# Kernel tuning notes

Hardware: AMD Instinct MI355X
Metric: run time of the kernel (lower is better)

## Reference

```python
import jax, jax.numpy as jnp
import numpy as np
from jax import lax

B, S, D, N_ORIG, GROUP_DIM, R = 8, 4096, 512, 4096, 64, 1024
EPS_MERGE = 1e-8
EPS_NORM = 1e-12  # F.normalize eps


def setup_inputs() -> dict:
    key = jax.random.key(0)
    k1, k2, k3 = jax.random.split(key, 3)
    x = jax.random.normal(k1, (B, S, D), dtype=jnp.float32)
    source = jax.random.normal(k2, (B, S, N_ORIG), dtype=jnp.float32)
    position_ids = jnp.arange(B * S, dtype=jnp.int32).reshape(B, S)
    # nn.Linear(dim, group_dim, bias=False) weight: (group_dim, dim)
    W = jax.random.normal(k3, (GROUP_DIM, D), dtype=jnp.float32) / np.sqrt(D)
    return {"x": x, "source": source, "position_ids": position_ids, "W": W, "r": R}


def _greedy_select(sim, r):
    """Greedy disjoint adjacent-pair selection; returns bool (S-1,) edge mask."""
    Sm1 = sim.shape[0]
    order = jnp.argsort(-sim, stable=True)  # matches torch.argsort(-sim, stable=True)

    def step(carry, p):
        used, sel, cnt = carry
        ok = (~used[p]) & (~used[p + 1]) & (cnt < r)
        used = used.at[p].set(used[p] | ok)
        used = used.at[p + 1].set(used[p + 1] | ok)
        sel = sel.at[p].set(ok)
        return (used, sel, cnt + ok.astype(jnp.int32)), None

    init = (jnp.zeros(Sm1 + 1, dtype=bool), jnp.zeros(Sm1, dtype=bool), jnp.int32(0))
    (_, sel, _), _ = lax.scan(step, init, order)
    return sel


def _merge_one(x, src, pos, sim, norms, r):
    Sl = x.shape[0]
    sel = _greedy_select(sim, r)  # sel[p] True => merge pair (p, p+1)
    w = norms[:, None]
    # weighted merge of adjacent pairs, written at position i = p
    merged = (w[:-1] * x[:-1] + w[1:] * x[1:]) / (w[:-1] + w[1:] + EPS_MERGE)
    x_out = jnp.concatenate([jnp.where(sel[:, None], merged, x[:-1]), x[-1:]], axis=0)
    src_out = src.at[:-1].add(jnp.where(sel[:, None], src[1:], 0.0))
    drop = jnp.concatenate([jnp.zeros(1, dtype=bool), sel])  # token p+1 dropped
    idx = jnp.arange(Sl)
    keep_order = jnp.argsort(jnp.where(drop, Sl + idx, idx))[: Sl - r]  # kept, in order
    return x_out[keep_order], src_out[keep_order], pos[keep_order]


def reference(x, source, position_ids, W, r):
    g = jnp.einsum("bsd,gd->bsg", x, W)  # group projection
    gnorms = jnp.linalg.norm(g, axis=-1)  # (B, S)
    g_unit = g / jnp.maximum(gnorms[..., None], EPS_NORM)
    sim = jnp.sum(g_unit[:, :-1] * g_unit[:, 1:], axis=-1)  # (B, S-1)
    merge = lambda xb, sb, pb, simb, nb: _merge_one(xb, sb, pb, simb, nb, r)
    return jax.vmap(merge)(x, source, position_ids, sim, gnorms)
```

## Files before the change

kernel.cpp:

```cpp
#include <hip/hip_runtime.h>
#include <hip/hip_bf16.h>
#include <stdint.h>

#define B_ 8
#define S_ 4096
#define D_ 512
#define G_ 64
#define R_ 1024
#define NO_ 4096
#define SO_ 3072
#define EPS_MERGE 1e-8f
#define EPS_NORM 1e-12f

typedef float f4v __attribute__((ext_vector_type(4)));

#define WS_G     0ull
#define WS_GN    8388608ull
#define WS_KEYS  8519680ull
#define WS_KEPT  8781824ull

__global__ __launch_bounds__(256) void k1_proj(const float* __restrict__ x,
                                               const float* __restrict__ W,
                                               float* __restrict__ g,
                                               float* __restrict__ gn) {
  __shared__ float xs[32][132];
  __shared__ float wc[32][68];
  const int tid = threadIdx.x;
  const int gt  = tid & 15;
  const int rt  = tid >> 4;
  const int rb  = blockIdx.x * 128;
  const int g0  = gt * 4;
  const int r0  = rt * 8;
  const int kq4 = (tid & 7) * 4;
  const int rl0 = tid >> 3;

  const float* xp[4];
  const float* wp[2];
#pragma unroll
  for (int i = 0; i < 4; ++i)
    xp[i] = &x[(size_t)(rb + rl0 + i * 32) * D_ + kq4];
#pragma unroll
  for (int i = 0; i < 2; ++i)
    wp[i] = &W[(size_t)(rl0 + i * 32) * D_ + kq4];

  float4 px[4], pw[2];
#pragma unroll
  for (int i = 0; i < 4; ++i) px[i] = *reinterpret_cast<const float4*>(xp[i]);
#pragma unroll
  for (int i = 0; i < 2; ++i) pw[i] = *reinterpret_cast<const float4*>(wp[i]);

  float acc[8][4];
#pragma unroll
  for (int r = 0; r < 8; ++r)
#pragma unroll
    for (int j = 0; j < 4; ++j) acc[r][j] = 0.f;

  for (int kc = 0; kc < 16; ++kc) {
    __syncthreads();
#pragma unroll
    for (int i = 0; i < 4; ++i) {
      const int rl = rl0 + i * 32;
      xs[kq4 + 0][rl] = px[i].x;
      xs[kq4 + 1][rl] = px[i].y;
      xs[kq4 + 2][rl] = px[i].z;
      xs[kq4 + 3][rl] = px[i].w;
    }
#pragma unroll
    for (int i = 0; i < 2; ++i) {
      const int gg = rl0 + i * 32;
      wc[kq4 + 0][gg] = pw[i].x;
      wc[kq4 + 1][gg] = pw[i].y;
      wc[kq4 + 2][gg] = pw[i].z;
      wc[kq4 + 3][gg] = pw[i].w;
    }
    if (kc < 15) {
      const int off = (kc + 1) * 32;
#pragma unroll
      for (int i = 0; i < 4; ++i)
        px[i] = *reinterpret_cast<const float4*>(xp[i] + off);
#pragma unroll
      for (int i = 0; i < 2; ++i)
        pw[i] = *reinterpret_cast<const float4*>(wp[i] + off);
    }
    __syncthreads();
#pragma unroll
    for (int k = 0; k < 32; ++k) {
      const float4 wv = *reinterpret_cast<const float4*>(&wc[k][g0]);
      const float4 xa = *reinterpret_cast<const float4*>(&xs[k][r0]);
      const float4 xb = *reinterpret_cast<const float4*>(&xs[k][r0 + 4]);
      const float xr[8] = {xa.x, xa.y, xa.z, xa.w, xb.x, xb.y, xb.z, xb.w};
#pragma unroll
      for (int r = 0; r < 8; ++r) {
        acc[r][0] = fmaf(xr[r], wv.x, acc[r][0]);
        acc[r][1] = fmaf(xr[r], wv.y, acc[r][1]);
        acc[r][2] = fmaf(xr[r], wv.z, acc[r][2]);
        acc[r][3] = fmaf(xr[r], wv.w, acc[r][3]);
      }
    }
  }
#pragma unroll
  for (int r = 0; r < 8; ++r) {
    const int row = rb + r0 + r;
    float4 v;
    v.x = acc[r][0]; v.y = acc[r][1]; v.z = acc[r][2]; v.w = acc[r][3];
    *reinterpret_cast<float4*>(&g[(size_t)row * G_ + g0]) = v;
    float ss = v.x * v.x + v.y * v.y + v.z * v.z + v.w * v.w;
    ss += __shfl_xor(ss, 1);
    ss += __shfl_xor(ss, 2);
    ss += __shfl_xor(ss, 4);
    ss += __shfl_xor(ss, 8);
    if (gt == 0) gn[row] = sqrtf(ss);
  }
}

__global__ __launch_bounds__(256) void k2_sim(const float* __restrict__ g,
                                              const float* __restrict__ gn,
                                              unsigned long long* __restrict__ prio) {
  const int wid = blockIdx.x * 4 + (threadIdx.x >> 6);
  const int lane = threadIdx.x & 63;
  if (wid >= B_ * (S_ - 1)) return;
  const int b = wid / (S_ - 1);
  const int e = wid - b * (S_ - 1);
  const size_t row = (size_t)b * S_ + e;
  const float a = g[row * G_ + lane];
  const float c = g[(row + 1) * G_ + lane];
  float p = a * c;
  p += __shfl_xor(p, 1);
  p += __shfl_xor(p, 2);
  p += __shfl_xor(p, 4);
  p += __shfl_xor(p, 8);
  p += __shfl_xor(p, 16);
  p += __shfl_xor(p, 32);
  if (lane == 0) {
    const float n0 = fmaxf(gn[row], EPS_NORM);
    const float n1 = fmaxf(gn[row + 1], EPS_NORM);
    const float sim = p / (n0 * n1);
    const unsigned int u = __float_as_uint(sim);
    const unsigned int m = (u & 0x80000000u) ? ~u : (u | 0x80000000u);
    prio[(size_t)b * S_ + e] =
        ((unsigned long long)m << 32) | (unsigned long long)(unsigned int)(4095 - e);
  }
}

__global__ __launch_bounds__(256) void k3_match(const unsigned long long* __restrict__ prio,
                                                unsigned int* __restrict__ kept) {
  __shared__ unsigned long long pr[4096];
  __shared__ unsigned int stw[258];
  __shared__ int hist[256];
  __shared__ int wsum[4];
  __shared__ int sh_flag;
  __shared__ int sh_need;
  __shared__ int sh_exact;
  __shared__ unsigned long long sh_prefix;
  __shared__ unsigned long long sh_tmin;
  __shared__ unsigned long long sh_tmax;

  const int tid = threadIdx.x;
  const int b = blockIdx.x;

#pragma unroll
  for (int j = 0; j < 16; ++j) {
    const int e = tid + j * 256;
    pr[e] = (e < 4095) ? prio[(size_t)b * S_ + e] : 0ull;
  }
  if (tid == 0) {
    stw[0] = 0xAAAAAAAAu;
    stw[257] = 0xAAAAAAAAu;
    sh_flag = 0; sh_need = R_; sh_prefix = 0ull;
    sh_exact = 0; sh_tmin = ~0ull; sh_tmax = 0ull;
  }
  stw[1 + tid] = (tid == 255) ? 0x80000000u : 0u;
  __syncthreads();

  unsigned int cl = 0, cr = 0;
#pragma unroll
  for (int j = 0; j < 16; ++j) {
    const int e = tid * 16 + j;
    const unsigned long long pe = pr[e];
    const bool L = (e == 0) || (pe > pr[e - 1]);
    const bool R = (e >= 4094) || (pe > pr[e + 1]);
    cl |= (L ? 1u : 0u) << (2 * j);
    cr |= (R ? 1u : 0u) << (2 * j);
  }

  for (;;) {
    __syncthreads();
    if (tid == 0) sh_flag = 0;
    __syncthreads();
    unsigned int u = stw[1 + tid];
    const unsigned int lw = stw[tid];
    const unsigned int rw = stw[2 + tid];
    const unsigned int linb = (lw >> 30) & 1u;
    const unsigned int loutb = (lw >> 31) & 1u;
    const unsigned int rinb = (rw & 1u) << 30;
    const unsigned int routb = ((rw >> 1) & 1u) << 30;
    bool changed = false;
    for (;;) {
      const unsigned int a = u & 0x55555555u;
      const unsigned int d = (u >> 1) & 0x55555555u;
      const unsigned int lin = (a << 2) | linb;
      const unsigned int lout = (d << 2) | loutb;
      const unsigned int rin = (a >> 2) | rinb;
      const unsigned int rout = (d >> 2) | routb;
      const unsigned int undec = ~(a | d) & 0x55555555u;
      const unsigned int nout = undec & (lin | rin);
      const unsigned int nin = undec & ~lin & ~rin & (lout | cl) & (rout | cr);
      if (!(nin | nout)) break;
      u |= nin | (nout << 1);
      changed = true;
    }
    if (changed) { stw[1 + tid] = u; sh_flag = 1; }
    __syncthreads();
    if (sh_flag == 0) break;
  }

  const unsigned int inw = stw[1 + tid] & 0x55555555u;

  int exitmode = 0;
#pragma unroll 1
  for (int level = 0; level < 8; ++level) {
    const int shift = 56 - 8 * level;
    __syncthreads();
    hist[tid] = 0;
    __syncthreads();
    const unsigned long long pref = sh_prefix;
#pragma unroll
    for (int j = 0; j < 16; ++j) {
      if (!((inw >> (2 * j)) & 1u)) continue;
      const unsigned long long p = pr[tid * 16 + j];
      const bool match = (level == 0) || ((p >> (shift + 8)) == (pref >> (shift + 8)));
      if (match) atomicAdd(&hist[(int)((p >> shift) & 255ull)], 1);
    }
    __syncthreads();
    if (tid < 64) {
      const int lane = tid;
      const int need = sh_need;
      const int h0 = hist[lane * 4 + 0], h1 = hist[lane * 4 + 1];
      const int h2 = hist[lane * 4 + 2], h3 = hist[lane * 4 + 3];
      const int gsum = h0 + h1 + h2 + h3;
      int s = gsum;
#pragma unroll
      for (int off = 1; off < 64; off <<= 1) {
        const int v = __shfl_down(s, off);
        if (lane + off < 64) s += v;
      }
      const int suffAbove = s - gsum;
      if (suffAbove < need && s >= need) {
        const int hh[4] = {h0, h1, h2, h3};
        int cum = suffAbove;
        for (int q = 3; q >= 0; --q) {
          cum += hh[q];
          if (cum >= need) {
            const int need2 = need - (cum - hh[q]);
            sh_prefix = pref | ((unsigned long long)(lane * 4 + q) << shift);
            sh_need = need2;
            if (need2 == hh[q]) sh_exact = 1;
            else if (need2 == 1) sh_exact = 2;
            break;
          }
        }
      }
    }
    __syncthreads();
    const int ex = sh_exact;
    if (ex) {
      exitmode = ex;
      const unsigned long long pref2 = sh_prefix;
      unsigned long long best = (ex == 1) ? ~0ull : 0ull;
#pragma unroll
      for (int j = 0; j < 16; ++j) {
        if (!((inw >> (2 * j)) & 1u)) continue;
        const unsigned long long p = pr[tid * 16 + j];
        if ((p >> shift) == (pref2 >> shift))
          best = (ex == 1) ? (best < p ? best : p) : (best > p ? best : p);
      }
#pragma unroll
      for (int off = 1; off < 64; off <<= 1) {
        const unsigned long long o = __shfl_xor(best, off);
        best = (ex == 1) ? (best < o ? best : o) : (best > o ? best : o);
      }
      if ((tid & 63) == 0) {
        if (ex == 1) atomicMin(&sh_tmin, best);
        else atomicMax(&sh_tmax, best);
      }
      __syncthreads();
      break;
    }
  }
  const unsigned long long thresh =
      (exitmode == 1) ? sh_tmin : (exitmode == 2) ? sh_tmax : sh_prefix;
  const unsigned int previnw = stw[tid] & 0x55555555u;

  int c = 0;
  unsigned int kpbits = 0;
#pragma unroll
  for (int j = 0; j < 16; ++j) {
    const int s = tid * 16 + j;
    bool selprev = false;
    if (s > 0) {
      const unsigned int ib =
          (j == 0) ? ((previnw >> 30) & 1u) : ((inw >> (2 * (j - 1))) & 1u);
      selprev = ib && (pr[s - 1] >= thresh);
    }
    if (!selprev) { kpbits |= 1u << j; ++c; }
  }
  const int lane = tid & 63, w = tid >> 6;
  int v = c;
#pragma unroll
  for (int off = 1; off < 64; off <<= 1) {
    const int t2 = __shfl_up(v, off);
    if (lane >= off) v += t2;
  }
  if (lane == 63) wsum[w] = v;
  __syncthreads();
  if (tid == 0) {
    int run = 0;
    for (int q = 0; q < 4; ++q) { const int t3 = wsum[q]; wsum[q] = run; run += t3; }
  }
  __syncthreads();
  int pos = (v - c) + wsum[w];
#pragma unroll
  for (int j = 0; j < 16; ++j) {
    if ((kpbits >> j) & 1u) {
      const int s = tid * 16 + j;
      const unsigned int m =
          (((inw >> (2 * j)) & 1u) && pr[s] >= thresh) ? 0x80000000u : 0u;
      kept[b * SO_ + pos] = (unsigned int)s | m;
      ++pos;
    }
  }
}

__global__ __launch_bounds__(256) void k45_gather(const float* __restrict__ src,
                                                  const float* __restrict__ x,
                                                  const float* __restrict__ gn,
                                                  const int* __restrict__ posid,
                                                  const unsigned int* __restrict__ kept,
                                                  float* __restrict__ outs,
                                                  float* __restrict__ outx,
                                                  float* __restrict__ outpos) {
  const int blk = blockIdx.x;
  const int b = blk / SO_;
  const int j = blk - b * SO_;
  const unsigned int ent = kept[b * SO_ + j];
  const int s = (int)(ent & 0x7FFFFFFFu);
  const bool m = (ent & 0x80000000u) != 0u;
  const size_t rrow = (size_t)b * S_ + s;
  const size_t orow = (size_t)b * SO_ + j;
  const size_t rin = rrow * NO_;
  const size_t rout = orow * NO_;
  const int t = threadIdx.x;

#pragma unroll
  for (int it = 0; it < 4; ++it) {
    const int f4 = t + it * 256;
    f4v a = __builtin_nontemporal_load(
        reinterpret_cast<const f4v*>(&src[rin + (size_t)f4 * 4]));
    if (m) {
      const f4v c2 = __builtin_nontemporal_load(
          reinterpret_cast<const f4v*>(&src[rin + NO_ + (size_t)f4 * 4]));
      a += c2;
    }
    __builtin_nontemporal_store(a, reinterpret_cast<f4v*>(&outs[rout + (size_t)f4 * 4]));
  }

  if (t < 128) {
    float4 a = *reinterpret_cast<const float4*>(&x[rrow * D_ + t * 4]);
    float4 o;
    if (m) {
      const float w0 = gn[rrow], w1 = gn[rrow + 1];
      const float4 c2 = *reinterpret_cast<const float4*>(&x[(rrow + 1) * D_ + t * 4]);
      const float den = w0 + w1 + EPS_MERGE;
      o.x = (w0 * a.x + w1 * c2.x) / den;
      o.y = (w0 * a.y + w1 * c2.y) / den;
      o.z = (w0 * a.z + w1 * c2.z) / den;
      o.w = (w0 * a.w + w1 * c2.w) / den;
    } else {
      o = a;
    }
    *reinterpret_cast<float4*>(&outx[orow * D_ + t * 4]) = o;
  }
  if (t == 0) outpos[orow] = (float)posid[rrow];
}

extern "C" void kernel_launch(void* const* d_in, const int* in_sizes, int n_in,
                              void* d_out, int out_size, void* d_ws, size_t ws_size,
                              hipStream_t stream) {
  (void)in_sizes; (void)n_in; (void)out_size; (void)ws_size;
  const float* x = (const float*)d_in[0];
  const float* src = (const float*)d_in[1];
  const int* posid = (const int*)d_in[2];
  const float* W = (const float*)d_in[3];

  char* ws = (char*)d_ws;
  float* g = (float*)(ws + WS_G);
  float* gn = (float*)(ws + WS_GN);
  unsigned long long* prio = (unsigned long long*)(ws + WS_KEYS);
  unsigned int* kept = (unsigned int*)(ws + WS_KEPT);

  float* outx = (float*)d_out;
  float* outs = outx + (size_t)B_ * SO_ * D_;
  float* outpos = outs + (size_t)B_ * SO_ * NO_;

  hipLaunchKernelGGL(k1_proj, dim3(256), dim3(256), 0, stream, x, W, g, gn);
  hipLaunchKernelGGL(k2_sim, dim3((B_ * (S_ - 1) + 3) / 4), dim3(256), 0, stream, g, gn, prio);
  hipLaunchKernelGGL(k3_match, dim3(B_), dim3(256), 0, stream, prio, kept);
  hipLaunchKernelGGL(k45_gather, dim3(B_ * SO_), dim3(256), 0, stream, src, x, gn,
                     posid, kept, outs, outx, outpos);
}
```

Measured before the change: 228.8 us.

## Fuse projection and similarity kernels, keep group projections in shared memory

Merges the projection GEMM and the adjacent-pair cosine similarity into one kernel. The projected tile stays in LDS, and one halo row from the next block is recomputed so edges at block boundaries can be scored locally. This removes the global write and read of the 8 MB g buffer and one kernel launch, at the cost of a small redundant row computation done by a few threads. It also switches the x loads and outx stores in the gather kernel to nontemporal access.

```diff
diff --git a/kernel.cpp b/kernel.cpp
--- a/kernel.cpp
+++ b/kernel.cpp
@@ -14,17 +14,18 @@
 
 typedef float f4v __attribute__((ext_vector_type(4)));
 
-#define WS_G     0ull
-#define WS_GN    8388608ull
-#define WS_KEYS  8519680ull
-#define WS_KEPT  8781824ull
-
-__global__ __launch_bounds__(256) void k1_proj(const float* __restrict__ x,
-                                               const float* __restrict__ W,
-                                               float* __restrict__ g,
-                                               float* __restrict__ gn) {
-  __shared__ float xs[32][132];
-  __shared__ float wc[32][68];
+#define WS_GN    0ull
+#define WS_KEYS  131072ull
+#define WS_KEPT  393216ull
+
+__global__ __launch_bounds__(256) void k12_proj_sim(const float* __restrict__ x,
+                                                    const float* __restrict__ W,
+                                                    float* __restrict__ gn,
+                                                    unsigned long long* __restrict__ prio) {
+  __shared__ union {
+    struct { float xs[32][132]; float wc[32][68]; } s;
+    float gs[129][66];
+  } u;
   const int tid = threadIdx.x;
   const int gt  = tid & 15;
   const int rt  = tid >> 4;
@@ -42,36 +43,46 @@
 #pragma unroll
   for (int i = 0; i < 2; ++i)
     wp[i] = &W[(size_t)(rl0 + i * 32) * D_ + kq4];
-
-  float4 px[4], pw[2];
+  const int rowB = (rb + 128 < B_ * S_) ? rb + 128 : B_ * S_ - 1;
+  const float* xbp = &x[(size_t)rowB * D_ + tid * 4];
+
+  float4 px[4], pw[2], pxb;
 #pragma unroll
   for (int i = 0; i < 4; ++i) px[i] = *reinterpret_cast<const float4*>(xp[i]);
 #pragma unroll
   for (int i = 0; i < 2; ++i) pw[i] = *reinterpret_cast<const float4*>(wp[i]);
+  if (tid < 8) pxb = *reinterpret_cast<const float4*>(xbp);
 
   float acc[8][4];
 #pragma unroll
   for (int r = 0; r < 8; ++r)
 #pragma unroll
     for (int j = 0; j < 4; ++j) acc[r][j] = 0.f;
+  float accB[4] = {0.f, 0.f, 0.f, 0.f};
 
   for (int kc = 0; kc < 16; ++kc) {
     __syncthreads();
 #pragma unroll
     for (int i = 0; i < 4; ++i) {
       const int rl = rl0 + i * 32;
-      xs[kq4 + 0][rl] = px[i].x;
-      xs[kq4 + 1][rl] = px[i].y;
-      xs[kq4 + 2][rl] = px[i].z;
-      xs[kq4 + 3][rl] = px[i].w;
+      u.s.xs[kq4 + 0][rl] = px[i].x;
+      u.s.xs[kq4 + 1][rl] = px[i].y;
+      u.s.xs[kq4 + 2][rl] = px[i].z;
+      u.s.xs[kq4 + 3][rl] = px[i].w;
     }
 #pragma unroll
     for (int i = 0; i < 2; ++i) {
       const int gg = rl0 + i * 32;
-      wc[kq4 + 0][gg] = pw[i].x;
-      wc[kq4 + 1][gg] = pw[i].y;
-      wc[kq4 + 2][gg] = pw[i].z;
-      wc[kq4 + 3][gg] = pw[i].w;
+      u.s.wc[kq4 + 0][gg] = pw[i].x;
+      u.s.wc[kq4 + 1][gg] = pw[i].y;
+      u.s.wc[kq4 + 2][gg] = pw[i].z;
+      u.s.wc[kq4 + 3][gg] = pw[i].w;
+    }
+    if (tid < 8) {
+      u.s.xs[tid * 4 + 0][128] = pxb.x;
+      u.s.xs[tid * 4 + 1][128] = pxb.y;
+      u.s.xs[tid * 4 + 2][128] = pxb.z;
+      u.s.xs[tid * 4 + 3][128] = pxb.w;
     }
     if (kc < 15) {
       const int off = (kc + 1) * 32;
@@ -81,13 +92,14 @@
 #pragma unroll
       for (int i = 0; i < 2; ++i)
         pw[i] = *reinterpret_cast<const float4*>(wp[i] + off);
+      if (tid < 8) pxb = *reinterpret_cast<const float4*>(xbp + off);
     }
     __syncthreads();
 #pragma unroll
     for (int k = 0; k < 32; ++k) {
-      const float4 wv = *reinterpret_cast<const float4*>(&wc[k][g0]);
-      const float4 xa = *reinterpret_cast<const float4*>(&xs[k][r0]);
-      const float4 xb = *reinterpret_cast<const float4*>(&xs[k][r0 + 4]);
+      const float4 wv = *reinterpret_cast<const float4*>(&u.s.wc[k][g0]);
+      const float4 xa = *reinterpret_cast<const float4*>(&u.s.xs[k][r0]);
+      const float4 xb = *reinterpret_cast<const float4*>(&u.s.xs[k][r0 + 4]);
       const float xr[8] = {xa.x, xa.y, xa.z, xa.w, xb.x, xb.y, xb.z, xb.w};
 #pragma unroll
       for (int r = 0; r < 8; ++r) {
@@ -97,48 +109,78 @@
         acc[r][3] = fmaf(xr[r], wv.w, acc[r][3]);
       }
     }
-  }
+    if (tid < 16) {
+#pragma unroll
+      for (int k = 0; k < 32; ++k) {
+        const float xb1 = u.s.xs[k][128];
+        const float4 wv = *reinterpret_cast<const float4*>(&u.s.wc[k][tid * 4]);
+        accB[0] = fmaf(xb1, wv.x, accB[0]);
+        accB[1] = fmaf(xb1, wv.y, accB[1]);
+        accB[2] = fmaf(xb1, wv.z, accB[2]);
+        accB[3] = fmaf(xb1, wv.w, accB[3]);
+      }
+    }
+  }
+
+  __syncthreads();
+
 #pragma unroll
   for (int r = 0; r < 8; ++r) {
-    const int row = rb + r0 + r;
+    const int rl = r0 + r;
     float4 v;
     v.x = acc[r][0]; v.y = acc[r][1]; v.z = acc[r][2]; v.w = acc[r][3];
-    *reinterpret_cast<float4*>(&g[(size_t)row * G_ + g0]) = v;
+    *reinterpret_cast<float4*>(&u.gs[rl][g0]) = v;
     float ss = v.x * v.x + v.y * v.y + v.z * v.z + v.w * v.w;
     ss += __shfl_xor(ss, 1);
     ss += __shfl_xor(ss, 2);
     ss += __shfl_xor(ss, 4);
     ss += __shfl_xor(ss, 8);
-    if (gt == 0) gn[row] = sqrtf(ss);
-  }
-}
-
-__global__ __launch_bounds__(256) void k2_sim(const float* __restrict__ g,
-                                              const float* __restrict__ gn,
-                                              unsigned long long* __restrict__ prio) {
-  const int wid = blockIdx.x * 4 + (threadIdx.x >> 6);
-  const int lane = threadIdx.x & 63;
-  if (wid >= B_ * (S_ - 1)) return;
-  const int b = wid / (S_ - 1);
-  const int e = wid - b * (S_ - 1);
-  const size_t row = (size_t)b * S_ + e;
-  const float a = g[row * G_ + lane];
-  const float c = g[(row + 1) * G_ + lane];
-  float p = a * c;
-  p += __shfl_xor(p, 1);
-  p += __shfl_xor(p, 2);
-  p += __shfl_xor(p, 4);
-  p += __shfl_xor(p, 8);
-  p += __shfl_xor(p, 16);
-  p += __shfl_xor(p, 32);
-  if (lane == 0) {
-    const float n0 = fmaxf(gn[row], EPS_NORM);
-    const float n1 = fmaxf(gn[row + 1], EPS_NORM);
-    const float sim = p / (n0 * n1);
-    const unsigned int u = __float_as_uint(sim);
-    const unsigned int m = (u & 0x80000000u) ? ~u : (u | 0x80000000u);
-    prio[(size_t)b * S_ + e] =
-        ((unsigned long long)m << 32) | (unsigned long long)(unsigned int)(4095 - e);
+    if (gt == 0) {
+      const float nv = sqrtf(ss);
+      gn[rb + rl] = nv;
+      u.gs[rl][64] = nv;
+    }
+  }
+  if (tid < 16) {
+    *reinterpret_cast<float4*>(&u.gs[128][tid * 4]) =
+        make_float4(accB[0], accB[1], accB[2], accB[3]);
+    float ss = accB[0] * accB[0] + accB[1] * accB[1] +
+               accB[2] * accB[2] + accB[3] * accB[3];
+    ss += __shfl_xor(ss, 1);
+    ss += __shfl_xor(ss, 2);
+    ss += __shfl_xor(ss, 4);
+    ss += __shfl_xor(ss, 8);
+    if (tid == 0) u.gs[128][64] = sqrtf(ss);
+  }
+  __syncthreads();
+
+  const int lastLe = ((rb & (S_ - 1)) == S_ - 128) ? 126 : 127;
+  const int wv_ = tid >> 6, lane = tid & 63;
+  const int bb = rb >> 12;
+  const int e0 = rb & (S_ - 1);
+#pragma unroll 2
+  for (int i = 0; i < 32; ++i) {
+    const int le = wv_ * 32 + i;
+    if (le > lastLe) break;
+    const float a = u.gs[le][lane];
+    const float c = u.gs[le + 1][lane];
+    float p = a * c;
+    p += __shfl_xor(p, 1);
+    p += __shfl_xor(p, 2);
+    p += __shfl_xor(p, 4);
+    p += __shfl_xor(p, 8);
+    p += __shfl_xor(p, 16);
+    p += __shfl_xor(p, 32);
+    if (lane == 0) {
+      const float n0 = fmaxf(u.gs[le][64], EPS_NORM);
+      const float n1 = fmaxf(u.gs[le + 1][64], EPS_NORM);
+      const float sim = p / (n0 * n1);
+      const unsigned int uu = __float_as_uint(sim);
+      const unsigned int mm = (uu & 0x80000000u) ? ~uu : (uu | 0x80000000u);
+      const int e = e0 + le;
+      prio[(size_t)bb * S_ + e] =
+          ((unsigned long long)mm << 32) | (unsigned long long)(unsigned int)(4095 - e);
+    }
   }
 }
 
@@ -365,11 +407,13 @@
   }
 
   if (t < 128) {
-    float4 a = *reinterpret_cast<const float4*>(&x[rrow * D_ + t * 4]);
-    float4 o;
+    f4v a = __builtin_nontemporal_load(
+        reinterpret_cast<const f4v*>(&x[rrow * D_ + t * 4]));
+    f4v o;
     if (m) {
       const float w0 = gn[rrow], w1 = gn[rrow + 1];
-      const float4 c2 = *reinterpret_cast<const float4*>(&x[(rrow + 1) * D_ + t * 4]);
+      const f4v c2 = __builtin_nontemporal_load(
+          reinterpret_cast<const f4v*>(&x[(rrow + 1) * D_ + t * 4]));
       const float den = w0 + w1 + EPS_MERGE;
       o.x = (w0 * a.x + w1 * c2.x) / den;
       o.y = (w0 * a.y + w1 * c2.y) / den;
@@ -378,7 +422,7 @@
     } else {
       o = a;
     }
-    *reinterpret_cast<float4*>(&outx[orow * D_ + t * 4]) = o;
+    __builtin_nontemporal_store(o, reinterpret_cast<f4v*>(&outx[orow * D_ + t * 4]));
   }
   if (t == 0) outpos[orow] = (float)posid[rrow];
 }
@@ -393,7 +437,6 @@
   const float* W = (const float*)d_in[3];
 
   char* ws = (char*)d_ws;
-  float* g = (float*)(ws + WS_G);
   float* gn = (float*)(ws + WS_GN);
   unsigned long long* prio = (unsigned long long*)(ws + WS_KEYS);
   unsigned int* kept = (unsigned int*)(ws + WS_KEPT);
@@ -402,8 +445,7 @@
   float* outs = outx + (size_t)B_ * SO_ * D_;
   float* outpos = outs + (size_t)B_ * SO_ * NO_;
 
-  hipLaunchKernelGGL(k1_proj, dim3(256), dim3(256), 0, stream, x, W, g, gn);
-  hipLaunchKernelGGL(k2_sim, dim3((B_ * (S_ - 1) + 3) / 4), dim3(256), 0, stream, g, gn, prio);
+  hipLaunchKernelGGL(k12_proj_sim, dim3(256), dim3(256), 0, stream, x, W, gn, prio);
   hipLaunchKernelGGL(k3_match, dim3(B_), dim3(256), 0, stream, prio, kept);
   hipLaunchKernelGGL(k45_gather, dim3(B_ * SO_), dim3(256), 0, stream, src, x, gn,
                      posid, kept, outs, outx, outpos);
```

New measurement: 364.2 us. +59.2%, slower.
